# Optimization experiments

Hardware: AMD Instinct MI355X
Metric: run time of the kernel (lower is better)

Reference implementation:

```python
import jax, jax.numpy as jnp
import numpy as np
from jax import lax

ANGLES = (0, 90, 180, 270)

def _conv(x, w, b, stride):
    # x: NCHW, w: OIHW, VALID padding (matches typical torch Conv2d defaults here)
    y = lax.conv_general_dilated(x, w, (stride, stride), 'VALID',
                                 dimension_numbers=('NCHW', 'OIHW', 'NCHW'))
    return y + b[None, :, None, None]

def setup_inputs() -> dict:
    key = jax.random.key(0)
    ks = jax.random.split(key, 11)
    B, C, H, W = 64, 3, 128, 128
    obs = jax.random.uniform(ks[0], (B, C, H, W), dtype=jnp.float32)
    s = lambda *sh: 1.0 / np.sqrt(np.prod(sh[1:]))
    w1 = jax.random.normal(ks[1], (32, 3, 8, 8), jnp.float32) * s(32, 3, 8, 8)
    b1 = jnp.zeros((32,), jnp.float32)
    w2 = jax.random.normal(ks[2], (64, 32, 4, 4), jnp.float32) * s(64, 32, 4, 4)
    b2 = jnp.zeros((64,), jnp.float32)
    w3 = jax.random.normal(ks[3], (64, 64, 3, 3), jnp.float32) * s(64, 64, 3, 3)
    b3 = jnp.zeros((64,), jnp.float32)
    # spatial after convs: 128 -> 31 -> 14 -> 12 ; flatten = 64*12*12 = 9216
    n_feat = 64 * 12 * 12
    fc1_w = jax.random.normal(ks[4], (512, n_feat), jnp.float32) * (1.0 / np.sqrt(n_feat))
    fc1_b = jnp.zeros((512,), jnp.float32)
    fc2_w = jax.random.normal(ks[5], (len(ANGLES), 512), jnp.float32) * (1.0 / np.sqrt(512))
    fc2_b = jnp.zeros((len(ANGLES),), jnp.float32)
    return dict(obs=obs, w1=w1, b1=b1, w2=w2, b2=b2, w3=w3, b3=b3,
                fc1_w=fc1_w, fc1_b=fc1_b, fc2_w=fc2_w, fc2_b=fc2_b)

def reference(obs, w1, b1, w2, b2, w3, b3, fc1_w, fc1_b, fc2_w, fc2_b):
    B = obs.shape[0]
    # Batched replacement for the per-sample cv2.warpAffine loop:
    # 90-degree CCW multiples on square images == exact rot90 permutation.
    rotated = jnp.concatenate(
        [jnp.rot90(obs, k=a // 90, axes=(2, 3)) for a in ANGLES], axis=0)
    labels = jnp.repeat(jnp.arange(len(ANGLES)), B).astype(jnp.float32)
    # Encoder (Nature-DQN style CNN)
    h = jax.nn.relu(_conv(rotated, w1, b1, 4))
    h = jax.nn.relu(_conv(h, w2, b2, 2))
    h = jax.nn.relu(_conv(h, w3, b3, 1))
    h = h.reshape(h.shape[0], -1)  # [4B, 9216]
    # Decoder MLP
    h = jax.nn.relu(h @ fc1_w.T + fc1_b)
    logits = h @ fc2_w.T + fc2_b  # [4B, n_angles]
    return logits, labels, rotated
```

## Files before the change

### kernel.cpp

```cpp
#include <hip/hip_runtime.h>


typedef short bf16x8 __attribute__((ext_vector_type(8)));
typedef float f32x4  __attribute__((ext_vector_type(4)));

__device__ __forceinline__ ushort f2bf(float f) {
    uint u = __float_as_uint(f);
    u += 0x7fffu + ((u >> 16) & 1u);
    return (ushort)(u >> 16);
}

__device__ __forceinline__ void nt_store4(float* p, f32x4 v) {
    __builtin_nontemporal_store(v, (f32x4*)p);
}

__device__ __forceinline__ void gload16(const void* g, void* l) {
    __builtin_amdgcn_global_load_lds(
        (const __attribute__((address_space(1))) unsigned int*)g,
        (__attribute__((address_space(3))) unsigned int*)l, 16, 0, 0);
}

__global__ __launch_bounds__(256) void prep_w1r(const float* __restrict__ w1,
                                                ushort* __restrict__ w1r,
                                                float* __restrict__ lab)
{
    const int bx = blockIdx.x, t = threadIdx.x;
    if (bx < 96) {
        int i = bx * 256 + t;
        int n = i / 192, r = i - n * 192;
        int ic = r >> 6, a8 = (r >> 3) & 7, b8 = r & 7;
        int a = n >> 5, oc = n & 31;
        int kh, kw;
        switch (a) {
            case 0:  kh = a8;     kw = b8;     break;
            case 1:  kh = 7 - b8; kw = a8;     break;
            case 2:  kh = 7 - a8; kw = 7 - b8; break;
            default: kh = b8;     kw = 7 - a8; break;
        }
        w1r[i] = f2bf(w1[((oc * 3 + ic) * 8 + kh) * 8 + kw]);
    } else {
        lab[t] = (float)(t >> 6);
    }
}

__global__ __launch_bounds__(256) void mega(const float* __restrict__ obs,
                                            const ushort* __restrict__ w1r,
                                            const float* __restrict__ b1,
                                            const float* __restrict__ fc1_w,
                                            const float* __restrict__ w2,
                                            const float* __restrict__ w3,
                                            float* __restrict__ rot,
                                            ushort* __restrict__ act1,
                                            ushort* __restrict__ fc1wr,
                                            ushort* __restrict__ w2r,
                                            ushort* __restrict__ w3r)
{
    __shared__ __align__(16) char smem[37120];
    const int bx = blockIdx.x, t = threadIdx.x;

    if (bx < 481) {
        ushort* aT = (ushort*)smem;
        ushort* bT = (ushort*)(smem + 16384);
        const int m0  = bx * 128;
        const int wid = t >> 6, l = t & 63;
        const int lrow = l & 15, lk = (l >> 4) << 3;
        const int wm = (wid >> 1) * 64, wn = (wid & 1) * 64;

        int abase[4], aoff[4], bbase[4];
        #pragma unroll
        for (int j = 0; j < 4; ++j) {
            int cid = j * 256 + t;
            int row = cid >> 3, c = cid & 7;
            int m = m0 + row; m = m < 61504 ? m : 61503;
            int b = m / 961; int rem = m - b * 961;
            int p = rem / 31; int q = rem - p * 31;
            abase[j] = ((b * 3) << 14) + ((p * 4 + c) << 7) + q * 4;
            aoff[j]  = (row * 64 + c * 8) ^ ((row & 7) << 3);
            bbase[j] = row * 192 + c * 8;
        }

        f32x4 acc[4][4] = {};
        for (int ic = 0; ic < 3; ++ic) {
            #pragma unroll
            for (int j = 0; j < 4; ++j) {
                const float* src = obs + abase[j] + (ic << 14);
                float4 v0 = *(const float4*)src;
                float4 v1 = *(const float4*)(src + 4);
                bf16x8 pk;
                pk[0] = (short)f2bf(v0.x); pk[1] = (short)f2bf(v0.y);
                pk[2] = (short)f2bf(v0.z); pk[3] = (short)f2bf(v0.w);
                pk[4] = (short)f2bf(v1.x); pk[5] = (short)f2bf(v1.y);
                pk[6] = (short)f2bf(v1.z); pk[7] = (short)f2bf(v1.w);
                *(bf16x8*)&aT[aoff[j]] = pk;
            }
            #pragma unroll
            for (int j = 0; j < 4; ++j)
                *(bf16x8*)&bT[aoff[j]] = *(const bf16x8*)&w1r[bbase[j] + ic * 64];
            __syncthreads();
            #pragma unroll
            for (int s = 0; s < 2; ++s) {
                bf16x8 af[4], bv[4];
                #pragma unroll
                for (int m = 0; m < 4; ++m) {
                    int r = wm + m * 16 + lrow;
                    af[m] = *(const bf16x8*)&aT[(r * 64 + s * 32 + lk) ^ ((r & 7) << 3)];
                }
                #pragma unroll
                for (int n = 0; n < 4; ++n) {
                    int r = wn + n * 16 + lrow;
                    bv[n] = *(const bf16x8*)&bT[(r * 64 + s * 32 + lk) ^ ((r & 7) << 3)];
                }
                #pragma unroll
                for (int m = 0; m < 4; ++m)
                    #pragma unroll
                    for (int n = 0; n < 4; ++n)
                        acc[m][n] = __builtin_amdgcn_mfma_f32_16x16x32_bf16(af[m], bv[n], acc[m][n], 0, 0, 0);
            }
            __syncthreads();
        }
        #pragma unroll
        for (int m = 0; m < 4; ++m)
            #pragma unroll
            for (int j = 0; j < 4; ++j) {
                int row = m0 + wm + m * 16 + ((l >> 4) << 2) + j;
                if (row < 61504) {
                    int b = row / 961; int rem = row - b * 961;
                    int p = rem / 31;  int q = rem - p * 31;
                    #pragma unroll
                    for (int n = 0; n < 4; ++n) {
                        int col = wn + n * 16 + lrow;
                        int a = col >> 5, oc = col & 31;
                        int oh, ow;
                        switch (a) {
                            case 0:  oh = p;      ow = q;      break;
                            case 1:  oh = 30 - q; ow = p;      break;
                            case 2:  oh = 30 - p; ow = 30 - q; break;
                            default: oh = q;      ow = 30 - p; break;
                        }
                        float v = acc[m][n][j] + b1[oc];
                        v = v > 0.f ? v : 0.f;
                        act1[(((a << 6) + b) * 961 + oh * 31 + ow) * 32 + oc] = f2bf(v);
                    }
                }
            }
    } else if (bx < 993) {
        float* s = (float*)smem;
        const int n = bx - 481;
        #pragma unroll
        for (int j = 0; j < 9; ++j) {
            int i = (j * 256 + t) * 4;
            float4 v = *(const float4*)&fc1_w[n * 9216 + i];
            int ic = i / 144, p = i - ic * 144;
            s[ic * 145 + p + 0] = v.x; s[ic * 145 + p + 1] = v.y;
            s[ic * 145 + p + 2] = v.z; s[ic * 145 + p + 3] = v.w;
        }
        __syncthreads();
        uint* op = (uint*)(fc1wr + n * 9216);
        #pragma unroll
        for (int j = 0; j < 18; ++j) {
            int q  = j * 256 + t;
            int jj = q * 2;
            int ic = jj & 63, p = jj >> 6;
            uint lo = f2bf(s[ic * 145 + p]);
            uint hi = f2bf(s[(ic + 1) * 145 + p]);
            op[q] = lo | (hi << 16);
        }
    } else if (bx < 4065) {
        float (*sN)[36] = (float(*)[36])smem;
        float (*sT)[33] = (float(*)[33])(smem + 4608);
        const int bb   = bx - 993;
        const int tile = bb & 15;
        const int cimg = bb >> 4;
        const int c = cimg % 3, b = cimg / 3;
        const int h0s = (tile >> 2) * 32, w0s = (tile & 3) * 32;
        const int rs = t >> 3, w4 = (t & 7) * 4;

        const float* src = obs + ((b * 3 + c) << 14);
        f32x4 v = *(const f32x4*)&src[((h0s + rs) << 7) + w0s + w4];
        *(f32x4*)&sN[rs][w4] = v;
        sT[w4 + 0][rs] = v.x; sT[w4 + 1][rs] = v.y;
        sT[w4 + 2][rs] = v.z; sT[w4 + 3][rs] = v.w;

        float* d0 = rot + (((      b) * 3 + c) << 14);
        float* d1 = rot + ((( 64 + b) * 3 + c) << 14);
        float* d2 = rot + (((128 + b) * 3 + c) << 14);
        float* d3 = rot + (((192 + b) * 3 + c) << 14);

        nt_store4(&d0[((h0s + rs) << 7) + w0s + w4], v);
        __syncthreads();
        f32x4 o;
        o.x = sT[31 - rs][w4 + 0]; o.y = sT[31 - rs][w4 + 1];
        o.z = sT[31 - rs][w4 + 2]; o.w = sT[31 - rs][w4 + 3];
        nt_store4(&d1[((96 - w0s + rs) << 7) + h0s + w4], o);
        o.x = sN[31 - rs][31 - w4 - 0]; o.y = sN[31 - rs][31 - w4 - 1];
        o.z = sN[31 - rs][31 - w4 - 2]; o.w = sN[31 - rs][31 - w4 - 3];
        nt_store4(&d2[((96 - h0s + rs) << 7) + (96 - w0s) + w4], o);
        o.x = sT[rs][31 - w4 - 0]; o.y = sT[rs][31 - w4 - 1];
        o.z = sT[rs][31 - w4 - 2]; o.w = sT[rs][31 - w4 - 3];
        nt_store4(&d3[((w0s + rs) << 7) + (96 - h0s) + w4], o);
    } else if (bx < 4193) {
        int i = (bx - 4065) * 256 + t;
        int ic = i & 31, kw = (i >> 5) & 3, kh = (i >> 7) & 3, oc = i >> 9;
        w2r[i] = f2bf(w2[((oc * 32 + ic) * 4 + kh) * 4 + kw]);
    } else {
        int i = (bx - 4193) * 256 + t;
        int ic = i & 63, r = i >> 6;
        int kw = r % 3, r2 = r / 3;
        int kh = r2 % 3, oc = r2 / 3;
        w3r[i] = f2bf(w3[((oc * 64 + ic) * 3 + kh) * 3 + kw]);
    }
}

template<int IC, int IH, int IW, int KH, int KW, int S, int OH, int OW>
__global__ __launch_bounds__(256) void conv_mfma(const ushort* __restrict__ in,
                                                 const ushort* __restrict__ wr,
                                                 const float* __restrict__ bias,
                                                 ushort* __restrict__ out)
{
    constexpr int BK  = KW * IC;
    constexpr int NCH = BK / 8;
    constexpr int AJ  = 128 * NCH / 256;
    constexpr int BJ  = 64 * NCH / 256;
    __shared__ __align__(16) ushort aT[128 * BK];
    __shared__ __align__(16) ushort bT[64 * BK];
    const int t  = threadIdx.x;
    const int m0 = blockIdx.x * 128;
    const int wid = t >> 6, l = t & 63;
    const int lrow = l & 15, lk = (l >> 4) << 3;

    int asrc[AJ], bsrc[BJ];
    #pragma unroll
    for (int j = 0; j < AJ; ++j) {
        int tau = j * 256 + t;
        int row = tau / NCH, c = tau - row * NCH;
        int m   = m0 + row;
        int n   = m / (OH * OW); int rem = m - n * (OH * OW);
        int oh  = rem / OW; int ow = rem - oh * OW;
        asrc[j] = ((n * IH + oh * S) * IW + ow * S) * IC + (c ^ (row & 7)) * 8;
    }
    #pragma unroll
    for (int j = 0; j < BJ; ++j) {
        int tau = j * 256 + t;
        int row = tau / NCH, c = tau - row * NCH;
        bsrc[j] = row * (KH * BK) + (c ^ (row & 7)) * 8;
    }

    f32x4 acc[2][4] = {};
    for (int kh = 0; kh < KH; ++kh) {
        #pragma unroll
        for (int j = 0; j < AJ; ++j)
            gload16(in + asrc[j] + kh * (IW * IC), aT + (j * 256 + t) * 8);
        #pragma unroll
        for (int j = 0; j < BJ; ++j)
            gload16(wr + bsrc[j] + kh * BK, bT + (j * 256 + t) * 8);
        __syncthreads();
        #pragma unroll
        for (int s = 0; s < BK / 32; ++s) {
            bf16x8 af[2], bv[4];
            #pragma unroll
            for (int m = 0; m < 2; ++m) {
                int r = wid * 32 + m * 16 + lrow;
                af[m] = *(const bf16x8*)&aT[(r * BK + s * 32 + lk) ^ ((r & 7) << 3)];
            }
            #pragma unroll
            for (int n = 0; n < 4; ++n) {
                int r = n * 16 + lrow;
                bv[n] = *(const bf16x8*)&bT[(r * BK + s * 32 + lk) ^ ((r & 7) << 3)];
            }
            #pragma unroll
            for (int m = 0; m < 2; ++m)
                #pragma unroll
                for (int n = 0; n < 4; ++n)
                    acc[m][n] = __builtin_amdgcn_mfma_f32_16x16x32_bf16(af[m], bv[n], acc[m][n], 0, 0, 0);
        }
        __syncthreads();
    }
    #pragma unroll
    for (int m = 0; m < 2; ++m)
        #pragma unroll
        for (int n = 0; n < 4; ++n)
            #pragma unroll
            for (int j = 0; j < 4; ++j) {
                int row = m0 + wid * 32 + m * 16 + ((l >> 4) << 2) + j;
                int col = n * 16 + lrow;
                float v = acc[m][n][j] + bias[col];
                v = v > 0.f ? v : 0.f;
                out[row * 64 + col] = f2bf(v);
            }
}

__global__ __launch_bounds__(256) void fc1_mfma(const ushort* __restrict__ A,
                                                const ushort* __restrict__ W,
                                                float* __restrict__ hpart)
{
    __shared__ __align__(16) ushort aT[64 * 64];
    __shared__ __align__(16) ushort bT[64 * 64];
    const int t  = threadIdx.x;
    const int m0 = blockIdx.x * 64, n0 = blockIdx.y * 64;
    const int z  = blockIdx.z;
    const int kb = z * 1152;
    const int wid = t >> 6, l = t & 63;
    const int lrow = l & 15, lk = (l >> 4) << 3;
    const int wm = (wid >> 1) * 32, wn = (wid & 1) * 32;

    int asrcb[2], bsrcb[2];
    #pragma unroll
    for (int j = 0; j < 2; ++j) {
        int tau = j * 256 + t;
        int row = tau >> 3, c = tau & 7;
        int csw = (c ^ (row & 7)) * 8;
        asrcb[j] = (m0 + row) * 9216 + kb + csw;
        bsrcb[j] = (n0 + row) * 9216 + kb + csw;
    }

    f32x4 acc[2][2] = {};
    for (int k0 = 0; k0 < 1152; k0 += 64) {
        #pragma unroll
        for (int j = 0; j < 2; ++j)
            gload16(A + asrcb[j] + k0, aT + (j * 256 + t) * 8);
        #pragma unroll
        for (int j = 0; j < 2; ++j)
            gload16(W + bsrcb[j] + k0, bT + (j * 256 + t) * 8);
        __syncthreads();
        #pragma unroll
        for (int s = 0; s < 2; ++s) {
            bf16x8 af[2], bv[2];
            #pragma unroll
            for (int m = 0; m < 2; ++m) {
                int r = wm + m * 16 + lrow;
                af[m] = *(const bf16x8*)&aT[(r * 64 + s * 32 + lk) ^ ((r & 7) << 3)];
            }
            #pragma unroll
            for (int n = 0; n < 2; ++n) {
                int r = wn + n * 16 + lrow;
                bv[n] = *(const bf16x8*)&bT[(r * 64 + s * 32 + lk) ^ ((r & 7) << 3)];
            }
            #pragma unroll
            for (int m = 0; m < 2; ++m)
                #pragma unroll
                for (int n = 0; n < 2; ++n)
                    acc[m][n] = __builtin_amdgcn_mfma_f32_16x16x32_bf16(af[m], bv[n], acc[m][n], 0, 0, 0);
        }
        __syncthreads();
    }
    #pragma unroll
    for (int m = 0; m < 2; ++m)
        #pragma unroll
        for (int n = 0; n < 2; ++n)
            #pragma unroll
            for (int j = 0; j < 4; ++j) {
                int row = m0 + wm + m * 16 + ((l >> 4) << 2) + j;
                int col = n0 + wn + n * 16 + lrow;
                hpart[(z * 256 + row) * 512 + col] = acc[m][n][j];
            }
}

__global__ __launch_bounds__(256) void fc2_kernel(const float* __restrict__ hp,
                                                  const float* __restrict__ b1,
                                                  const float* __restrict__ W2,
                                                  const float* __restrict__ b2,
                                                  float* __restrict__ logits)
{
    __shared__ float s[512];
    const int i = blockIdx.x;
    const int t = threadIdx.x;
    for (int k = t; k < 512; k += 256) {
        float v = b1[k];
        #pragma unroll
        for (int z = 0; z < 8; ++z) v += hp[(z * 256 + i) * 512 + k];
        s[k] = v > 0.f ? v : 0.f;
    }
    __syncthreads();
    const int j = t >> 6;
    const int l = t & 63;
    float p = 0.f;
    #pragma unroll
    for (int q = 0; q < 8; ++q) p += s[l + q * 64] * W2[j * 512 + l + q * 64];
    #pragma unroll
    for (int off = 32; off > 0; off >>= 1) p += __shfl_xor(p, off);
    if (l == 0) logits[i * 4 + j] = p + b2[j];
}

extern "C" void kernel_launch(void* const* d_in, const int* in_sizes, int n_in,
                              void* d_out, int out_size, void* d_ws, size_t ws_size,
                              hipStream_t stream)
{
    const float* obs   = (const float*)d_in[0];
    const float* w1    = (const float*)d_in[1];
    const float* b1    = (const float*)d_in[2];
    const float* w2    = (const float*)d_in[3];
    const float* b2    = (const float*)d_in[4];
    const float* w3    = (const float*)d_in[5];
    const float* b3    = (const float*)d_in[6];
    const float* fc1_w = (const float*)d_in[7];
    const float* fc1_b = (const float*)d_in[8];
    const float* fc2_w = (const float*)d_in[9];
    const float* fc2_b = (const float*)d_in[10];

    float* out    = (float*)d_out;
    float* logits = out;
    float* labels = out + 1024;
    float* rot    = out + 1280;

    char* ws = (char*)d_ws;
    ushort* act1  = (ushort*)(ws);
    ushort* act2  = (ushort*)(ws + 15745024);
    ushort* act3  = (ushort*)(ws + 22167552);
    ushort* w2r   = (ushort*)(ws + 26886144);
    ushort* w3r   = (ushort*)(ws + 26951680);
    ushort* fc1wr = (ushort*)(ws + 27025408);
    float*  hpart = (float*) (ws + 36462592);
    ushort* w1r   = (ushort*)(ws + 40656896);

    prep_w1r<<<97, 256, 0, stream>>>(w1, w1r, labels);

    mega<<<4337, 256, 0, stream>>>(obs, w1r, b1, fc1_w, w2, w3,
                                   rot, act1, fc1wr, w2r, w3r);

    conv_mfma<32, 31, 31, 4, 4, 2, 14, 14><<<392, 256, 0, stream>>>(act1, w2r, b2, act2);
    conv_mfma<64, 14, 14, 3, 3, 1, 12, 12><<<288, 256, 0, stream>>>(act2, w3r, b3, act3);

    fc1_mfma<<<dim3(4, 8, 8), 256, 0, stream>>>(act3, fc1wr, hpart);
    fc2_kernel<<<256, 256, 0, stream>>>(hpart, fc1_b, fc2_w, fc2_b, logits);
}
```

Before: 65.34 us.

## Pre-convert obs to bf16 and stream conv1 tiles via direct global-to-LDS loads

A prep kernel now converts the whole fp32 observation tensor to bf16 in workspace, reusing the act2 region. The conv1 GEMM in the mega kernel then loads its A and B tiles straight into LDS with global_load_lds, using a swizzled source column instead of a swizzled LDS destination. This removes the per-tile fp32 loads, the register conversion and the LDS writes from the conv1 loop. In exchange there is an extra full pass over obs (fp32 read, bf16 write) in a separate kernel before conv1.

```diff
diff --git a/kernel.cpp b/kernel.cpp
--- a/kernel.cpp
+++ b/kernel.cpp
@@ -20,9 +20,11 @@
         (__attribute__((address_space(3))) unsigned int*)l, 16, 0, 0);
 }
 
-__global__ __launch_bounds__(256) void prep_w1r(const float* __restrict__ w1,
-                                                ushort* __restrict__ w1r,
-                                                float* __restrict__ lab)
+__global__ __launch_bounds__(256) void prep0(const float* __restrict__ w1,
+                                             const float* __restrict__ obs,
+                                             ushort* __restrict__ w1r,
+                                             float* __restrict__ lab,
+                                             ushort* __restrict__ bobs)
 {
     const int bx = blockIdx.x, t = threadIdx.x;
     if (bx < 96) {
@@ -38,12 +40,23 @@
             default: kh = b8;     kw = 7 - a8; break;
         }
         w1r[i] = f2bf(w1[((oc * 3 + ic) * 8 + kh) * 8 + kw]);
+    } else if (bx == 96) {
+        lab[t] = (float)(t >> 6);
     } else {
-        lab[t] = (float)(t >> 6);
+        int i = (bx - 97) * 2048 + t * 8;
+        float4 v0 = *(const float4*)&obs[i];
+        float4 v1 = *(const float4*)&obs[i + 4];
+        bf16x8 pk;
+        pk[0] = (short)f2bf(v0.x); pk[1] = (short)f2bf(v0.y);
+        pk[2] = (short)f2bf(v0.z); pk[3] = (short)f2bf(v0.w);
+        pk[4] = (short)f2bf(v1.x); pk[5] = (short)f2bf(v1.y);
+        pk[6] = (short)f2bf(v1.z); pk[7] = (short)f2bf(v1.w);
+        *(bf16x8*)&bobs[i] = pk;
     }
 }
 
 __global__ __launch_bounds__(256) void mega(const float* __restrict__ obs,
+                                            const ushort* __restrict__ bobs,
                                             const ushort* __restrict__ w1r,
                                             const float* __restrict__ b1,
                                             const float* __restrict__ fc1_w,
@@ -66,36 +79,27 @@
         const int lrow = l & 15, lk = (l >> 4) << 3;
         const int wm = (wid >> 1) * 64, wn = (wid & 1) * 64;
 
-        int abase[4], aoff[4], bbase[4];
+        int asrc[4], bsrc[4];
         #pragma unroll
         for (int j = 0; j < 4; ++j) {
             int cid = j * 256 + t;
             int row = cid >> 3, c = cid & 7;
+            int cs  = c ^ (row & 7);
             int m = m0 + row; m = m < 61504 ? m : 61503;
             int b = m / 961; int rem = m - b * 961;
             int p = rem / 31; int q = rem - p * 31;
-            abase[j] = ((b * 3) << 14) + ((p * 4 + c) << 7) + q * 4;
-            aoff[j]  = (row * 64 + c * 8) ^ ((row & 7) << 3);
-            bbase[j] = row * 192 + c * 8;
+            asrc[j] = ((b * 3) << 14) + ((p * 4 + cs) << 7) + q * 4;
+            bsrc[j] = row * 192 + cs * 8;
         }
 
         f32x4 acc[4][4] = {};
         for (int ic = 0; ic < 3; ++ic) {
             #pragma unroll
-            for (int j = 0; j < 4; ++j) {
-                const float* src = obs + abase[j] + (ic << 14);
-                float4 v0 = *(const float4*)src;
-                float4 v1 = *(const float4*)(src + 4);
-                bf16x8 pk;
-                pk[0] = (short)f2bf(v0.x); pk[1] = (short)f2bf(v0.y);
-                pk[2] = (short)f2bf(v0.z); pk[3] = (short)f2bf(v0.w);
-                pk[4] = (short)f2bf(v1.x); pk[5] = (short)f2bf(v1.y);
-                pk[6] = (short)f2bf(v1.z); pk[7] = (short)f2bf(v1.w);
-                *(bf16x8*)&aT[aoff[j]] = pk;
-            }
-            #pragma unroll
             for (int j = 0; j < 4; ++j)
-                *(bf16x8*)&bT[aoff[j]] = *(const bf16x8*)&w1r[bbase[j] + ic * 64];
+                gload16(bobs + asrc[j] + (ic << 14), aT + (j * 256 + t) * 8);
+            #pragma unroll
+            for (int j = 0; j < 4; ++j)
+                gload16(w1r + bsrc[j] + ic * 64, bT + (j * 256 + t) * 8);
             __syncthreads();
             #pragma unroll
             for (int s = 0; s < 2; ++s) {
@@ -405,6 +409,7 @@
     char* ws = (char*)d_ws;
     ushort* act1  = (ushort*)(ws);
     ushort* act2  = (ushort*)(ws + 15745024);
+    ushort* bobs  = (ushort*)(ws + 15745024);
     ushort* act3  = (ushort*)(ws + 22167552);
     ushort* w2r   = (ushort*)(ws + 26886144);
     ushort* w3r   = (ushort*)(ws + 26951680);
@@ -412,9 +417,9 @@
     float*  hpart = (float*) (ws + 36462592);
     ushort* w1r   = (ushort*)(ws + 40656896);
 
-    prep_w1r<<<97, 256, 0, stream>>>(w1, w1r, labels);
-
-    mega<<<4337, 256, 0, stream>>>(obs, w1r, b1, fc1_w, w2, w3,
+    prep0<<<1633, 256, 0, stream>>>(w1, obs, w1r, labels, bobs);
+
+    mega<<<4337, 256, 0, stream>>>(obs, bobs, w1r, b1, fc1_w, w2, w3,
                                    rot, act1, fc1wr, w2r, w3r);
 
     conv_mfma<32, 31, 31, 4, 4, 2, 14, 14><<<392, 256, 0, stream>>>(act1, w2r, b2, act2);
```

New measurement: 65.26 us. No clear change (-0.1%).
